# Kernel tuning notes

Hardware: AMD Instinct MI355X
Metric: run time of the kernel (lower is better)

## Reference

```python
import jax, jax.numpy as jnp
import numpy as np

D_QUERY = 512
D_AUDIO = 512
D_OUT = 512
B, HW, S = 16, 4096, 1024


def setup_inputs() -> dict:
    key = jax.random.key(0)
    ks = jax.random.split(key, 8)
    sc_q = 1.0 / np.sqrt(D_QUERY)
    sc_a = 1.0 / np.sqrt(D_AUDIO)
    return {
        "x": jax.random.normal(ks[0], (B, HW, D_QUERY), dtype=jnp.float32),
        "audio_embed": jax.random.normal(ks[1], (B, S, D_AUDIO), dtype=jnp.float32),
        "Wq": jax.random.uniform(ks[2], (D_QUERY, D_OUT), jnp.float32, -sc_q, sc_q),
        "bq": jax.random.uniform(ks[3], (D_OUT,), jnp.float32, -sc_q, sc_q),
        "Wk": jax.random.uniform(ks[4], (D_AUDIO, D_OUT), jnp.float32, -sc_a, sc_a),
        "bk": jax.random.uniform(ks[5], (D_OUT,), jnp.float32, -sc_a, sc_a),
        "Wv": jax.random.uniform(ks[6], (D_AUDIO, D_OUT), jnp.float32, -sc_a, sc_a),
        "bv": jax.random.uniform(ks[7], (D_OUT,), jnp.float32, -sc_a, sc_a),
    }


def reference(x, audio_embed, Wq, bq, Wk, bk, Wv, bv):
    # Linear projections (nn.Linear: y = x @ W^T + b; we store W already transposed)
    Q = x @ Wq + bq                      # [B, HW, D_OUT]
    K = audio_embed @ Wk + bk            # [B, S, D_OUT]
    V = audio_embed @ Wv + bv            # [B, S, D_OUT]
    scale = 1.0 / (K.shape[-1] ** 0.5)   # divide by sqrt(d_out), per source
    scores = jnp.einsum("bnd,bsd->bns", Q, K) * scale  # [B, HW, S]
    attn = jax.nn.softmax(scores, axis=-1)
    return jnp.einsum("bns,bsd->bnd", attn, V)         # [B, HW, D_OUT]
```

## Files before the change

### kernel.cpp

```cpp
#include <hip/hip_runtime.h>
#include <hip/hip_bf16.h>

typedef __attribute__((ext_vector_type(8))) short bf16x8;
typedef __attribute__((ext_vector_type(4))) float f32x4;
typedef __attribute__((ext_vector_type(4))) unsigned short ushort4v;

#define AS1 __attribute__((address_space(1)))
#define AS3 __attribute__((address_space(3)))

__device__ __forceinline__ float bf_bits_to_f(short s) {
  unsigned int u = ((unsigned int)(unsigned short)s) << 16;
  union { unsigned int u; float f; } c; c.u = u; return c.f;
}
__device__ __forceinline__ unsigned short f_to_bf_bits(float f) {
  union { float f; unsigned int u; } c; c.f = f;
  unsigned int r = c.u + 0x7FFFu + ((c.u >> 16) & 1u);
  return (unsigned short)(r >> 16);
}

__device__ __forceinline__ int fsw(int row) { return ((row >> 1) & 3) << 4; }

__global__ __launch_bounds__(256) void cvt_bf16_kernel(const float* __restrict__ in,
                                                       unsigned short* __restrict__ out,
                                                       long n) {
  const long nchunks = n >> 2;
  const long stride = (long)gridDim.x * 256;
  for (long c = (long)blockIdx.x * 256 + threadIdx.x; c < nchunks; c += stride) {
    f32x4 v = *(const f32x4*)(in + c * 4);
    ushort4v o;
    o[0] = f_to_bf_bits(v[0]); o[1] = f_to_bf_bits(v[1]);
    o[2] = f_to_bf_bits(v[2]); o[3] = f_to_bf_bits(v[3]);
    *(ushort4v*)(out + c * 4) = o;
  }
}

__global__ __launch_bounds__(256) void transpose_w_kernel(
    const float* __restrict__ W0, const float* __restrict__ W1, const float* __restrict__ W2,
    unsigned short* __restrict__ T0, unsigned short* __restrict__ T1, unsigned short* __restrict__ T2) {
  const float* W = (blockIdx.z == 0) ? W0 : (blockIdx.z == 1) ? W1 : W2;
  unsigned short* T = (blockIdx.z == 0) ? T0 : (blockIdx.z == 1) ? T1 : T2;
  __shared__ float t[32][33];
  const int tx = threadIdx.x & 31, ty = threadIdx.x >> 5;
  const int n0 = blockIdx.x * 32, k0 = blockIdx.y * 32;
#pragma unroll
  for (int j = 0; j < 4; ++j)
    t[ty + 8 * j][tx] = W[(long)(k0 + ty + 8 * j) * 512 + n0 + tx];
  __syncthreads();
#pragma unroll
  for (int j = 0; j < 4; ++j)
    T[(long)(n0 + ty + 8 * j) * 512 + k0 + tx] = f_to_bf_bits(t[tx][ty + 8 * j]);
}

template <bool BIAS, bool TRANSOUT, bool AFP32>
__global__ __launch_bounds__(256) void gemm_kernel(
    const void* __restrict__ Aptr,
    const unsigned short* __restrict__ BT,
    const float* __restrict__ bias,
    unsigned short* __restrict__ Cout,
    const int K, const float scale,
    const long strideA, const long strideBT, const long strideC, const int ldc,
    const int nx, const int ny) {
  __shared__ unsigned short lds[8192];
  const int nwg = gridDim.x;
  const int chunk = nwg >> 3;
  const int bid = blockIdx.x;
  const int swz = (bid & 7) * chunk + (bid >> 3);
  const int bx = swz % nx;
  const int t1 = swz / nx;
  const int by = t1 % ny;
  const int bz = t1 / ny;

  const int tid = threadIdx.x;
  const int lane = tid & 63;
  const int wv = tid >> 6;
  const int wr = wv >> 1, wc = wv & 1;
  const unsigned short* Ab = (const unsigned short*)Aptr + (long)bz * strideA + (long)by * 128 * K;
  const float* Af = (const float*)Aptr + (long)bz * strideA + (long)by * 128 * K;
  const unsigned short* Bb = BT + (long)bz * strideBT + (long)bx * 128 * K;

  f32x4 acc[4][4];
#pragma unroll
  for (int m = 0; m < 4; ++m)
#pragma unroll
    for (int n = 0; n < 4; ++n) acc[m][n] = (f32x4){0.f, 0.f, 0.f, 0.f};

  const int r15 = lane & 15, g = lane >> 4;
  const int kiters = K >> 5;
  const int asw = fsw(r15);

  int arow[2], acs[2];
#pragma unroll
  for (int i = 0; i < 2; ++i) {
    const int c = i * 4 + wv;
    const int boff = c * 1024 + lane * 16;
    arow[i] = boff >> 6;
    acs[i] = (boff & 63) ^ fsw(arow[i]);
  }
  f32x4 pa[2][2];
  if (AFP32) {
#pragma unroll
    for (int i = 0; i < 2; ++i) {
      const float* s = Af + (long)arow[i] * K + (acs[i] >> 1);
      pa[i][0] = *(const f32x4*)s;
      pa[i][1] = *(const f32x4*)(s + 4);
    }
  }

  for (int kt = 0; kt < kiters; ++kt) {
#pragma unroll
    for (int i = 0; i < 2; ++i) {
      const int c = i * 4 + wv;
      const char* srcB = (const char*)Bb + (long)arow[i] * (K * 2) + kt * 64 + acs[i];
      __builtin_amdgcn_global_load_lds(
          (const AS1 void*)srcB, (AS3 void*)(lds + 4096 + c * 512), 16, 0, 0);
      if (!AFP32) {
        const char* srcA = (const char*)Ab + (long)arow[i] * (K * 2) + kt * 64 + acs[i];
        __builtin_amdgcn_global_load_lds(
            (const AS1 void*)srcA, (AS3 void*)(lds + c * 512), 16, 0, 0);
      }
    }
    if (AFP32) {
#pragma unroll
      for (int i = 0; i < 2; ++i) {
        const int c = i * 4 + wv;
        bf16x8 w;
#pragma unroll
        for (int e = 0; e < 4; ++e) {
          w[e] = (short)f_to_bf_bits(pa[i][0][e]);
          w[4 + e] = (short)f_to_bf_bits(pa[i][1][e]);
        }
        *(bf16x8*)&lds[c * 512 + lane * 8] = w;
      }
      if (kt < kiters - 1) {
#pragma unroll
        for (int i = 0; i < 2; ++i) {
          const float* s = Af + (long)arow[i] * K + (kt + 1) * 32 + (acs[i] >> 1);
          pa[i][0] = *(const f32x4*)s;
          pa[i][1] = *(const f32x4*)(s + 4);
        }
      }
    }
    __syncthreads();

    bf16x8 af[4], bf[4];
#pragma unroll
    for (int m = 0; m < 4; ++m)
      af[m] = *(const bf16x8*)((const char*)lds + (wr * 64 + m * 16 + r15) * 64 + (g * 16 ^ asw));
#pragma unroll
    for (int n = 0; n < 4; ++n)
      bf[n] = *(const bf16x8*)((const char*)lds + 8192 +
                               (wc * 64 + n * 16 + r15) * 64 + (g * 16 ^ asw));
#pragma unroll
    for (int m = 0; m < 4; ++m)
#pragma unroll
      for (int n = 0; n < 4; ++n)
        acc[m][n] = __builtin_amdgcn_mfma_f32_16x16x32_bf16(af[m], bf[n], acc[m][n], 0, 0, 0);
    __syncthreads();
  }

  const long crow0 = (long)by * 128 + wr * 64;
  const long ccol0 = (long)bx * 128 + wc * 64;
#pragma unroll
  for (int n = 0; n < 4; ++n) {
    const long col = ccol0 + n * 16 + r15;
    const float bv = BIAS ? bias[col] : 0.f;
#pragma unroll
    for (int m = 0; m < 4; ++m) {
      const f32x4 v = acc[m][n];
#pragma unroll
      for (int j = 0; j < 4; ++j) {
        const long row = crow0 + m * 16 + g * 4 + j;
        const float val = (v[j] + bv) * scale;
        const long idx = TRANSOUT ? (col * (long)ldc + row) : (row * (long)ldc + col);
        (Cout + (long)bz * strideC)[idx] = f_to_bf_bits(val);
      }
    }
  }
}

template <bool EXPSTATS, bool DIVSTATS>
__global__ __launch_bounds__(512, 2) void gemm256_kernel(
    const unsigned short* __restrict__ A,
    const unsigned short* __restrict__ BT,
    void* __restrict__ Cout,
    const int K,
    const long strideA, const long strideBT, const long strideC, const int ldc,
    const int nx, const int ny, float* __restrict__ stats) {
  __shared__ __align__(16) char ldsb[4][32768];
  __shared__ float ssum[256][4];
  __shared__ float invl[256];

  const int nwg = gridDim.x;
  const int chunk = nwg >> 3;
  const int bid = blockIdx.x;
  const int swz = (bid & 7) * chunk + (bid >> 3);
  const int bx = swz % nx;
  const int t1 = swz / nx;
  const int by = t1 % ny;
  const int bz = t1 / ny;

  const int tid = threadIdx.x;
  const int lane = tid & 63;
  const int w = tid >> 6;
  const int wm = w >> 2, wn = w & 3;
  const int r15 = lane & 15, g = lane >> 4;

  const unsigned short* Ab = A + (long)bz * strideA + (long)by * 256 * K;
  const unsigned short* Bb = BT + (long)bz * strideBT + (long)bx * 256 * K;
  const int rowstride = K * 2;

  if (DIVSTATS) {
    if (tid < 256) {
      const f32x4 s = *(const f32x4*)&stats[((long)bz * 4096 + (long)by * 256 + tid) * 4];
      invl[tid] = 1.f / (s[0] + s[1] + s[2] + s[3]);
    }
  }

  const int boff0 = tid * 16;
  const int boff1 = 8192 + tid * 16;
  const int arow0 = boff0 >> 6;
  const int arow1 = boff1 >> 6;
  const int acs0 = (boff0 & 63) ^ fsw(arow0);
  const int acs1 = (boff1 & 63) ^ fsw(arow1);

  auto stage = [&](int kt2, int bsel) {
    char* dst = ldsb[bsel];
    const char* sA = (const char*)Ab + kt2 * 64;
    const char* sB = (const char*)Bb + kt2 * 64;
    __builtin_amdgcn_global_load_lds((const AS1 void*)(sA + (long)arow0 * rowstride + acs0),
                                     (AS3 void*)(dst + boff0), 16, 0, 0);
    __builtin_amdgcn_global_load_lds((const AS1 void*)(sB + (long)arow0 * rowstride + acs0),
                                     (AS3 void*)(dst + 16384 + boff0), 16, 0, 0);
    __builtin_amdgcn_global_load_lds((const AS1 void*)(sA + (long)arow1 * rowstride + acs1),
                                     (AS3 void*)(dst + boff1), 16, 0, 0);
    __builtin_amdgcn_global_load_lds((const AS1 void*)(sB + (long)arow1 * rowstride + acs1),
                                     (AS3 void*)(dst + 16384 + boff1), 16, 0, 0);
  };

  f32x4 acc[8][4];
#pragma unroll
  for (int m = 0; m < 8; ++m)
#pragma unroll
    for (int n = 0; n < 4; ++n) acc[m][n] = (f32x4){0.f, 0.f, 0.f, 0.f};

  const int kiters = K >> 5;
  const int asw = fsw(r15);
  stage(0, 0);
  stage(1, 1);
  stage(2, 2);

  for (int kt = 0; kt < kiters; ++kt) {
    if (kt < kiters - 2) {
      asm volatile("s_waitcnt vmcnt(8)" ::: "memory");
    } else if (kt == kiters - 2) {
      asm volatile("s_waitcnt vmcnt(4)" ::: "memory");
    } else {
      asm volatile("s_waitcnt vmcnt(0)" ::: "memory");
    }
    __builtin_amdgcn_s_barrier();
    __builtin_amdgcn_sched_barrier(0);
    if (kt + 3 < kiters) stage(kt + 3, (kt + 3) & 3);

    const char* bA = ldsb[kt & 3];
    const char* bB = ldsb[kt & 3] + 16384;
    bf16x8 af[8], bfr[4];
#pragma unroll
    for (int m = 0; m < 8; ++m)
      af[m] = *(const bf16x8*)(bA + (wm * 128 + m * 16 + r15) * 64 + (g * 16 ^ asw));
#pragma unroll
    for (int n = 0; n < 4; ++n)
      bfr[n] = *(const bf16x8*)(bB + (wn * 64 + n * 16 + r15) * 64 + (g * 16 ^ asw));

    __builtin_amdgcn_s_setprio(1);
#pragma unroll
    for (int m = 0; m < 8; ++m)
#pragma unroll
      for (int n = 0; n < 4; ++n)
        acc[m][n] = __builtin_amdgcn_mfma_f32_16x16x32_bf16(af[m], bfr[n], acc[m][n], 0, 0, 0);
    __builtin_amdgcn_s_setprio(0);
  }

  if (EXPSTATS) {
#pragma unroll
    for (int m = 0; m < 8; ++m)
#pragma unroll
      for (int n = 0; n < 4; ++n)
#pragma unroll
        for (int j = 0; j < 4; ++j) acc[m][n][j] = __expf(acc[m][n][j]);
#pragma unroll
    for (int m = 0; m < 8; ++m)
#pragma unroll
      for (int j = 0; j < 4; ++j) {
        float s = acc[m][0][j] + acc[m][1][j] + acc[m][2][j] + acc[m][3][j];
        s += __shfl_xor(s, 1);
        s += __shfl_xor(s, 2);
        s += __shfl_xor(s, 4);
        s += __shfl_xor(s, 8);
        if (r15 == 0) ssum[wm * 128 + m * 16 + g * 4 + j][wn] = s;
      }
    __syncthreads();
    if (tid < 256) {
      const float t = ssum[tid][0] + ssum[tid][1] + ssum[tid][2] + ssum[tid][3];
      stats[((long)bz * 4096 + (long)by * 256 + tid) * 4 + bx] = t;
    }
  }

  const long crow0 = (long)by * 256 + wm * 128;
  const long ccol0 = (long)bx * 256 + wn * 64;
#pragma unroll
  for (int m = 0; m < 8; ++m)
#pragma unroll
    for (int j = 0; j < 4; ++j) {
      const int rl = wm * 128 + m * 16 + g * 4 + j;
      const long row = crow0 + m * 16 + g * 4 + j;
#pragma unroll
      for (int n = 0; n < 4; ++n) {
        const long col = ccol0 + n * 16 + r15;
        if (EXPSTATS) {
          ((unsigned short*)Cout + (long)bz * strideC)[row * (long)ldc + col] =
              f_to_bf_bits(acc[m][n][j]);
        } else {
          const float sc = DIVSTATS ? invl[rl] : 1.f;
          ((float*)Cout + (long)bz * strideC)[row * (long)ldc + col] = acc[m][n][j] * sc;
        }
      }
    }
}

extern "C" void kernel_launch(void* const* d_in, const int* in_sizes, int n_in,
                              void* d_out, int out_size, void* d_ws, size_t ws_size,
                              hipStream_t stream) {
  (void)in_sizes; (void)n_in; (void)out_size; (void)ws_size;
  const float* x     = (const float*)d_in[0];
  const float* audio = (const float*)d_in[1];
  const float* Wq    = (const float*)d_in[2];
  const float* bq    = (const float*)d_in[3];
  const float* Wk    = (const float*)d_in[4];
  const float* bk    = (const float*)d_in[5];
  const float* Wv    = (const float*)d_in[6];
  const float* bv    = (const float*)d_in[7];
  float* out = (float*)d_out;

  char* ws = (char*)d_ws;
  size_t off = 0;
  auto carve = [&](size_t bytes) { char* p = ws + off; off += (bytes + 255) & ~(size_t)255; return p; };
  unsigned short* ab  = (unsigned short*)carve((size_t)16384 * 512 * 2);
  unsigned short* wqt = (unsigned short*)carve((size_t)512 * 512 * 2);
  unsigned short* wkt = (unsigned short*)carve((size_t)512 * 512 * 2);
  unsigned short* wvt = (unsigned short*)carve((size_t)512 * 512 * 2);
  unsigned short* Qb  = (unsigned short*)carve((size_t)65536 * 512 * 2);
  unsigned short* Kb  = (unsigned short*)carve((size_t)16384 * 512 * 2);
  unsigned short* Vt  = (unsigned short*)carve((size_t)16384 * 512 * 2);
  unsigned short* Pb  = (unsigned short*)carve((size_t)65536 * 1024 * 2);
  float*          ls  = (float*)carve((size_t)65536 * 4 * 4);

  cvt_bf16_kernel<<<1024, 256, 0, stream>>>(audio, ab, (long)16384 * 512);
  transpose_w_kernel<<<dim3(16, 16, 3), 256, 0, stream>>>(Wq, Wk, Wv, wqt, wkt, wvt);
  gemm_kernel<true, false, true><<<4 * 512, 256, 0, stream>>>(
      x, wqt, bq, Qb, 512, 0.044194173824159216f, 0, 0, 0, 512, 4, 512);
  gemm_kernel<true, false, false><<<4 * 128, 256, 0, stream>>>(
      ab, wkt, bk, Kb, 512, 1.f, 0, 0, 0, 512, 4, 128);
  gemm_kernel<true, true, false><<<4 * 8 * 16, 256, 0, stream>>>(
      ab, wvt, bv, Vt, 512, 1.f, (long)1024 * 512, 0, (long)512 * 1024, 1024, 4, 8);
  gemm256_kernel<true, false><<<4 * 16 * 16, 512, 0, stream>>>(
      Qb, Kb, Pb, 512,
      (long)4096 * 512, (long)1024 * 512, (long)4096 * 1024, 1024, 4, 16, ls);
  gemm256_kernel<false, true><<<2 * 16 * 16, 512, 0, stream>>>(
      Pb, Vt, out, 1024,
      (long)4096 * 1024, (long)512 * 1024, (long)4096 * 512, 512, 2, 16, ls);
}
```

Baseline: 367.3 us.

## Interleave GEMM main loop into four MFMA quadrants with staggered global-to-LDS loads

Replaces the 4-buffer, 3-deep prefetch ring with a 3-buffer, 2-deep ring. Each k-step is split into four quadrant phases separated by barriers. Each phase issues one global_load_lds, reads only the A/B fragments it needs, and runs 8 MFMAs, so the fragment reads and load issue are spread across the compute. This is meant to lower register pressure from holding all fragments at once, free LDS, and overlap memory traffic with MFMA more finely. The cost is four barriers per k-step instead of one, plus a shallower prefetch depth that could expose load latency.

Result: faster. 357.9 us (-2.6%).

```diff
diff --git a/kernel.cpp b/kernel.cpp
--- a/kernel.cpp
+++ b/kernel.cpp
@@ -186,7 +186,7 @@
     const int K,
     const long strideA, const long strideBT, const long strideC, const int ldc,
     const int nx, const int ny, float* __restrict__ stats) {
-  __shared__ __align__(16) char ldsb[4][32768];
+  __shared__ __align__(16) char ring[3][32768];
   __shared__ float ssum[256][4];
   __shared__ float invl[256];
 
@@ -207,7 +207,7 @@
 
   const unsigned short* Ab = A + (long)bz * strideA + (long)by * 256 * K;
   const unsigned short* Bb = BT + (long)bz * strideBT + (long)bx * 256 * K;
-  const int rowstride = K * 2;
+  const long rsb = (long)K * 2;
 
   if (DIVSTATS) {
     if (tid < 256) {
@@ -216,25 +216,17 @@
     }
   }
 
-  const int boff0 = tid * 16;
-  const int boff1 = 8192 + tid * 16;
-  const int arow0 = boff0 >> 6;
-  const int arow1 = boff1 >> 6;
-  const int acs0 = (boff0 & 63) ^ fsw(arow0);
-  const int acs1 = (boff1 & 63) ^ fsw(arow1);
-
-  auto stage = [&](int kt2, int bsel) {
-    char* dst = ldsb[bsel];
-    const char* sA = (const char*)Ab + kt2 * 64;
-    const char* sB = (const char*)Bb + kt2 * 64;
-    __builtin_amdgcn_global_load_lds((const AS1 void*)(sA + (long)arow0 * rowstride + acs0),
-                                     (AS3 void*)(dst + boff0), 16, 0, 0);
-    __builtin_amdgcn_global_load_lds((const AS1 void*)(sB + (long)arow0 * rowstride + acs0),
-                                     (AS3 void*)(dst + 16384 + boff0), 16, 0, 0);
-    __builtin_amdgcn_global_load_lds((const AS1 void*)(sA + (long)arow1 * rowstride + acs1),
-                                     (AS3 void*)(dst + boff1), 16, 0, 0);
-    __builtin_amdgcn_global_load_lds((const AS1 void*)(sB + (long)arow1 * rowstride + acs1),
-                                     (AS3 void*)(dst + 16384 + boff1), 16, 0, 0);
+  const int boff = tid * 16;
+  const int srow = boff >> 6;
+  const int scol = (boff & 63) ^ fsw(srow);
+  const long sOff0 = (long)srow * rsb + scol;
+  const long sOff1 = (long)(srow + 128) * rsb + scol;
+  const char* Abyt = (const char*)Ab;
+  const char* Bbyt = (const char*)Bb;
+
+  auto gl1 = [&](const char* srcBase, long srcOff, char* dstBase, int dstOff) {
+    __builtin_amdgcn_global_load_lds((const AS1 void*)(srcBase + srcOff),
+                                     (AS3 void*)(dstBase + dstOff), 16, 0, 0);
   };
 
   f32x4 acc[8][4];
@@ -245,39 +237,85 @@
 
   const int kiters = K >> 5;
   const int asw = fsw(r15);
-  stage(0, 0);
-  stage(1, 1);
-  stage(2, 2);
-
+
+  gl1(Abyt, sOff0, ring[0], boff);
+  gl1(Abyt, sOff1, ring[0], 8192 + boff);
+  gl1(Bbyt, sOff0, ring[0], 16384 + boff);
+  gl1(Bbyt, sOff1, ring[0], 24576 + boff);
+  gl1(Abyt, sOff0 + 64, ring[1], boff);
+  gl1(Abyt, sOff1 + 64, ring[1], 8192 + boff);
+  gl1(Bbyt, sOff0 + 64, ring[1], 16384 + boff);
+  gl1(Bbyt, sOff1 + 64, ring[1], 24576 + boff);
+
+  int cur = 0, sb = 2;
   for (int kt = 0; kt < kiters; ++kt) {
-    if (kt < kiters - 2) {
-      asm volatile("s_waitcnt vmcnt(8)" ::: "memory");
-    } else if (kt == kiters - 2) {
-      asm volatile("s_waitcnt vmcnt(4)" ::: "memory");
-    } else {
-      asm volatile("s_waitcnt vmcnt(0)" ::: "memory");
-    }
+    const char* bA = ring[cur];
+    const char* bB = ring[cur] + 16384;
+    char* sd = ring[sb];
+    const bool st = (kt + 2) < kiters;
+    const long kb = (long)(kt + 2) * 64;
+    bf16x8 af0[4], af1[4], bf0[2], bf1[2];
+
+    if (kt + 1 < kiters) asm volatile("s_waitcnt vmcnt(4)" ::: "memory");
+    else                 asm volatile("s_waitcnt vmcnt(0)" ::: "memory");
     __builtin_amdgcn_s_barrier();
     __builtin_amdgcn_sched_barrier(0);
-    if (kt + 3 < kiters) stage(kt + 3, (kt + 3) & 3);
-
-    const char* bA = ldsb[kt & 3];
-    const char* bB = ldsb[kt & 3] + 16384;
-    bf16x8 af[8], bfr[4];
-#pragma unroll
-    for (int m = 0; m < 8; ++m)
-      af[m] = *(const bf16x8*)(bA + (wm * 128 + m * 16 + r15) * 64 + (g * 16 ^ asw));
-#pragma unroll
-    for (int n = 0; n < 4; ++n)
-      bfr[n] = *(const bf16x8*)(bB + (wn * 64 + n * 16 + r15) * 64 + (g * 16 ^ asw));
-
+#pragma unroll
+    for (int m = 0; m < 4; ++m)
+      af0[m] = *(const bf16x8*)(bA + (wm * 128 + m * 16 + r15) * 64 + ((g * 16) ^ asw));
+#pragma unroll
+    for (int n = 0; n < 2; ++n)
+      bf0[n] = *(const bf16x8*)(bB + (wn * 64 + n * 16 + r15) * 64 + ((g * 16) ^ asw));
+    if (st) gl1(Abyt, sOff0 + kb, sd, boff);
     __builtin_amdgcn_s_setprio(1);
 #pragma unroll
-    for (int m = 0; m < 8; ++m)
-#pragma unroll
-      for (int n = 0; n < 4; ++n)
-        acc[m][n] = __builtin_amdgcn_mfma_f32_16x16x32_bf16(af[m], bfr[n], acc[m][n], 0, 0, 0);
+    for (int m = 0; m < 4; ++m)
+#pragma unroll
+      for (int n = 0; n < 2; ++n)
+        acc[m][n] = __builtin_amdgcn_mfma_f32_16x16x32_bf16(af0[m], bf0[n], acc[m][n], 0, 0, 0);
     __builtin_amdgcn_s_setprio(0);
+
+    __builtin_amdgcn_s_barrier();
+    __builtin_amdgcn_sched_barrier(0);
+#pragma unroll
+    for (int n = 0; n < 2; ++n)
+      bf1[n] = *(const bf16x8*)(bB + (wn * 64 + (n + 2) * 16 + r15) * 64 + ((g * 16) ^ asw));
+    if (st) gl1(Abyt, sOff1 + kb, sd, 8192 + boff);
+    __builtin_amdgcn_s_setprio(1);
+#pragma unroll
+    for (int m = 0; m < 4; ++m)
+#pragma unroll
+      for (int n = 0; n < 2; ++n)
+        acc[m][2 + n] = __builtin_amdgcn_mfma_f32_16x16x32_bf16(af0[m], bf1[n], acc[m][2 + n], 0, 0, 0);
+    __builtin_amdgcn_s_setprio(0);
+
+    __builtin_amdgcn_s_barrier();
+    __builtin_amdgcn_sched_barrier(0);
+#pragma unroll
+    for (int m = 0; m < 4; ++m)
+      af1[m] = *(const bf16x8*)(bA + (wm * 128 + (m + 4) * 16 + r15) * 64 + ((g * 16) ^ asw));
+    if (st) gl1(Bbyt, sOff0 + kb, sd, 16384 + boff);
+    __builtin_amdgcn_s_setprio(1);
+#pragma unroll
+    for (int m = 0; m < 4; ++m)
+#pragma unroll
+      for (int n = 0; n < 2; ++n)
+        acc[4 + m][2 + n] = __builtin_amdgcn_mfma_f32_16x16x32_bf16(af1[m], bf1[n], acc[4 + m][2 + n], 0, 0, 0);
+    __builtin_amdgcn_s_setprio(0);
+
+    __builtin_amdgcn_s_barrier();
+    __builtin_amdgcn_sched_barrier(0);
+    if (st) gl1(Bbyt, sOff1 + kb, sd, 24576 + boff);
+    __builtin_amdgcn_s_setprio(1);
+#pragma unroll
+    for (int m = 0; m < 4; ++m)
+#pragma unroll
+      for (int n = 0; n < 2; ++n)
+        acc[4 + m][n] = __builtin_amdgcn_mfma_f32_16x16x32_bf16(af1[m], bf0[n], acc[4 + m][n], 0, 0, 0);
+    __builtin_amdgcn_s_setprio(0);
+
+    cur = (cur == 2) ? 0 : cur + 1;
+    sb = (sb == 2) ? 0 : sb + 1;
   }
 
   if (EXPSTATS) {
```

## Restructure GEMM main loop to read LDS fragments before barrier and prefetch

Applied to the files above, without the earlier changes.

Reorders the 4-buffer GEMM pipeline: each iteration loads its A/B fragments from LDS first, then waits on outstanding global loads, barriers, and only then issues the next stage's global-to-LDS copies before the MFMAs. This hides LDS read latency behind the vmcnt wait and lets the barrier guard buffer reuse. The staging layout is also simplified so each thread copies one row slice at rows r and r+128, which changes address arithmetic. The prologue adds an explicit wait and barrier, and the main loop adds sched_barriers that constrain compiler scheduling.

After: 337.3 us. 1.09x faster.

```diff
diff --git a/kernel.cpp b/kernel.cpp
--- a/kernel.cpp
+++ b/kernel.cpp
@@ -186,7 +186,7 @@
     const int K,
     const long strideA, const long strideBT, const long strideC, const int ldc,
     const int nx, const int ny, float* __restrict__ stats) {
-  __shared__ __align__(16) char ldsb[4][32768];
+  __shared__ __align__(16) char halfb[4][32768];
   __shared__ float ssum[256][4];
   __shared__ float invl[256];
 
@@ -204,10 +204,11 @@
   const int w = tid >> 6;
   const int wm = w >> 2, wn = w & 3;
   const int r15 = lane & 15, g = lane >> 4;
-
-  const unsigned short* Ab = A + (long)bz * strideA + (long)by * 256 * K;
-  const unsigned short* Bb = BT + (long)bz * strideBT + (long)bx * 256 * K;
-  const int rowstride = K * 2;
+  const int asw = fsw(r15);
+
+  const char* Abyt = (const char*)(A + (long)bz * strideA + (long)by * 256 * K);
+  const char* Bbyt = (const char*)(BT + (long)bz * strideBT + (long)bx * 256 * K);
+  const long rsb = (long)K * 2;
 
   if (DIVSTATS) {
     if (tid < 256) {
@@ -215,26 +216,25 @@
       invl[tid] = 1.f / (s[0] + s[1] + s[2] + s[3]);
     }
   }
-
-  const int boff0 = tid * 16;
-  const int boff1 = 8192 + tid * 16;
-  const int arow0 = boff0 >> 6;
-  const int arow1 = boff1 >> 6;
-  const int acs0 = (boff0 & 63) ^ fsw(arow0);
-  const int acs1 = (boff1 & 63) ^ fsw(arow1);
-
-  auto stage = [&](int kt2, int bsel) {
-    char* dst = ldsb[bsel];
-    const char* sA = (const char*)Ab + kt2 * 64;
-    const char* sB = (const char*)Bb + kt2 * 64;
-    __builtin_amdgcn_global_load_lds((const AS1 void*)(sA + (long)arow0 * rowstride + acs0),
-                                     (AS3 void*)(dst + boff0), 16, 0, 0);
-    __builtin_amdgcn_global_load_lds((const AS1 void*)(sB + (long)arow0 * rowstride + acs0),
-                                     (AS3 void*)(dst + 16384 + boff0), 16, 0, 0);
-    __builtin_amdgcn_global_load_lds((const AS1 void*)(sA + (long)arow1 * rowstride + acs1),
-                                     (AS3 void*)(dst + boff1), 16, 0, 0);
-    __builtin_amdgcn_global_load_lds((const AS1 void*)(sB + (long)arow1 * rowstride + acs1),
-                                     (AS3 void*)(dst + 16384 + boff1), 16, 0, 0);
+  __builtin_amdgcn_sched_barrier(0);
+
+  const int srow0 = tid >> 2;
+  const int scol = ((tid & 3) << 4) ^ fsw(srow0);
+  const long aoff0 = (long)srow0 * rsb + scol;
+  const long aoff1 = (long)(srow0 + 128) * rsb + scol;
+  const int dbase = tid * 16;
+
+  auto stage = [&](int s) {
+    char* h = halfb[s & 3];
+    const long kb = (long)s * 64;
+    __builtin_amdgcn_global_load_lds((const AS1 void*)(Abyt + aoff0 + kb),
+                                     (AS3 void*)(h + dbase), 16, 0, 0);
+    __builtin_amdgcn_global_load_lds((const AS1 void*)(Abyt + aoff1 + kb),
+                                     (AS3 void*)(h + 8192 + dbase), 16, 0, 0);
+    __builtin_amdgcn_global_load_lds((const AS1 void*)(Bbyt + aoff0 + kb),
+                                     (AS3 void*)(h + 16384 + dbase), 16, 0, 0);
+    __builtin_amdgcn_global_load_lds((const AS1 void*)(Bbyt + aoff1 + kb),
+                                     (AS3 void*)(h + 24576 + dbase), 16, 0, 0);
   };
 
   f32x4 acc[8][4];
@@ -243,41 +243,40 @@
 #pragma unroll
     for (int n = 0; n < 4; ++n) acc[m][n] = (f32x4){0.f, 0.f, 0.f, 0.f};
 
-  const int kiters = K >> 5;
-  const int asw = fsw(r15);
-  stage(0, 0);
-  stage(1, 1);
-  stage(2, 2);
-
-  for (int kt = 0; kt < kiters; ++kt) {
-    if (kt < kiters - 2) {
-      asm volatile("s_waitcnt vmcnt(8)" ::: "memory");
-    } else if (kt == kiters - 2) {
-      asm volatile("s_waitcnt vmcnt(4)" ::: "memory");
-    } else {
-      asm volatile("s_waitcnt vmcnt(0)" ::: "memory");
-    }
+  const int kslices = K >> 5;
+
+  stage(0);
+  stage(1);
+  stage(2);
+  asm volatile("s_waitcnt vmcnt(8)" ::: "memory");
+  __builtin_amdgcn_s_barrier();
+  __builtin_amdgcn_sched_barrier(0);
+
+  for (int s = 0; s < kslices; ++s) {
+    const char* hA = halfb[s & 3];
+    const char* hB = halfb[s & 3] + 16384;
+    bf16x8 fa[8], fb[4];
+#pragma unroll
+    for (int m = 0; m < 8; ++m)
+      fa[m] = *(const bf16x8*)(hA + (wm * 128 + m * 16 + r15) * 64 + ((g * 16) ^ asw));
+#pragma unroll
+    for (int n = 0; n < 4; ++n)
+      fb[n] = *(const bf16x8*)(hB + (wn * 64 + n * 16 + r15) * 64 + ((g * 16) ^ asw));
+    __builtin_amdgcn_sched_barrier(0);
+    if (s < kslices - 2) asm volatile("s_waitcnt vmcnt(4)" ::: "memory");
+    else                 asm volatile("s_waitcnt vmcnt(0)" ::: "memory");
     __builtin_amdgcn_s_barrier();
+    asm volatile("s_waitcnt lgkmcnt(0)" ::: "memory");
     __builtin_amdgcn_sched_barrier(0);
-    if (kt + 3 < kiters) stage(kt + 3, (kt + 3) & 3);
-
-    const char* bA = ldsb[kt & 3];
-    const char* bB = ldsb[kt & 3] + 16384;
-    bf16x8 af[8], bfr[4];
+    if (s + 3 < kslices) stage(s + 3);
+    __builtin_amdgcn_s_setprio(1);
 #pragma unroll
     for (int m = 0; m < 8; ++m)
-      af[m] = *(const bf16x8*)(bA + (wm * 128 + m * 16 + r15) * 64 + (g * 16 ^ asw));
-#pragma unroll
-    for (int n = 0; n < 4; ++n)
-      bfr[n] = *(const bf16x8*)(bB + (wn * 64 + n * 16 + r15) * 64 + (g * 16 ^ asw));
-
-    __builtin_amdgcn_s_setprio(1);
-#pragma unroll
-    for (int m = 0; m < 8; ++m)
 #pragma unroll
       for (int n = 0; n < 4; ++n)
-        acc[m][n] = __builtin_amdgcn_mfma_f32_16x16x32_bf16(af[m], bfr[n], acc[m][n], 0, 0, 0);
+        acc[m][n] = __builtin_amdgcn_mfma_f32_16x16x32_bf16(fa[m], fb[n], acc[m][n], 0, 0, 0);
     __builtin_amdgcn_s_setprio(0);
+    __builtin_amdgcn_sched_barrier(0);
   }
 
   if (EXPSTATS) {
```
